# Kernel optimization log

Measured on AMD Instinct MI355X. Metric: run time of the kernel, lower is better.

The kernel has to match this reference:

```python
import jax, jax.numpy as jnp
import numpy as np

N = 100000
E = 1600000
IN_FEATS = 128
OUT_FEATS = 64


def setup_inputs() -> dict:
    key = jax.random.key(0)
    ks = jax.random.split(key, 8)
    node_feat = jax.random.normal(ks[0], (N, IN_FEATS), dtype=jnp.float32)
    edge_feat = jax.random.normal(ks[1], (E, 1), dtype=jnp.float32)
    # Linear params (PyTorch Linear: y = x @ W^T + b; we store W already transposed as [in, out])
    W_node = jax.random.normal(ks[2], (IN_FEATS, OUT_FEATS), dtype=jnp.float32) / np.sqrt(IN_FEATS)
    b_node = jax.random.normal(ks[3], (OUT_FEATS,), dtype=jnp.float32) * 0.01
    W_edge = jax.random.normal(ks[4], (1, OUT_FEATS), dtype=jnp.float32)
    b_edge = jax.random.normal(ks[5], (OUT_FEATS,), dtype=jnp.float32) * 0.01
    src = jax.random.randint(ks[6], (E,), 0, N, dtype=jnp.int32)
    dst = jax.random.randint(ks[7], (E,), 0, N, dtype=jnp.int32)
    return {"node_feat": node_feat, "edge_feat": edge_feat, "W_node": W_node,
            "b_node": b_node, "W_edge": W_edge, "b_edge": b_edge,
            "src": src, "dst": dst}


def reference(node_feat, edge_feat, W_node, b_node, W_edge, b_edge, src, dst):
    n_nodes = node_feat.shape[0]
    # node linear: h = node_fc(node_feat)  -> [N, out]
    h = node_feat @ W_node + b_node
    # edge linear: he = edge_fc(edge_feat) -> [E, out]
    he = edge_feat @ W_edge + b_edge
    # u_add_e: m = h[src] + he  (gather + add)  -> [E, out]
    m = h[src] + he
    # mean aggregate over destination nodes (segment mean; 0 for isolated nodes, as in DGL)
    msg_sum = jax.ops.segment_sum(m, dst, num_segments=n_nodes)  # [N, out]
    deg = jax.ops.segment_sum(jnp.ones((dst.shape[0],), dtype=m.dtype), dst, num_segments=n_nodes)  # [N]
    h_new = msg_sum / jnp.maximum(deg, 1.0)[:, None]
    return h_new
```

## Files before the change

kernel.cpp:

```cpp
#include <hip/hip_runtime.h>

#define IN_F 128
#define OUT_F 64
#define BSH 6
#define BNODES 64
#define NBMAX 1600
#define MSC 4096
#define CAPB 2048

typedef __attribute__((ext_vector_type(8))) short short8;
typedef __attribute__((ext_vector_type(4))) float f32x4;

static __device__ __forceinline__ unsigned short f2bf(float f) {
    unsigned u = __float_as_uint(f);
    u += 0x7FFF + ((u >> 16) & 1);
    return (unsigned short)(u >> 16);
}

__global__ void prep(const float* __restrict__ W, unsigned short* __restrict__ Wt,
                     int* __restrict__ gcur, int nb) {
    int i = blockIdx.x * 256 + threadIdx.x;
    if (i < OUT_F * IN_F) {
        int o = i >> 7, k = i & 127;
        Wt[i] = f2bf(W[k * OUT_F + o]);
    }
    if (i < nb) gcur[i] = i * CAPB;
}

__global__ __launch_bounds__(256) void node_linear_mfma(const float* __restrict__ nf,
                                                        const unsigned short* __restrict__ Wt,
                                                        const float* __restrict__ bn,
                                                        unsigned short* __restrict__ h16,
                                                        int n_nodes, int n_tiles) {
    const int lane = threadIdx.x & 63;
    const int wid  = threadIdx.x >> 6;
    const int l15  = lane & 15;
    const int kq   = lane >> 4;

    short8 bfrag[4][4];
#pragma unroll
    for (int c = 0; c < 4; ++c)
#pragma unroll
        for (int ks = 0; ks < 4; ++ks)
            bfrag[c][ks] = *(const short8*)&Wt[(c * 16 + l15) * IN_F + ks * 32 + kq * 8];

    float bv[4];
#pragma unroll
    for (int c = 0; c < 4; ++c) bv[c] = bn[c * 16 + l15];

    for (int tile = blockIdx.x * 4 + wid; tile < n_tiles; tile += gridDim.x * 4) {
        int arow = tile * 16 + l15;
        if (arow >= n_nodes) arow = n_nodes - 1;
        const float* rp = nf + (size_t)arow * IN_F + kq * 8;

        f32x4 acc[4];
#pragma unroll
        for (int c = 0; c < 4; ++c) acc[c] = (f32x4){bv[c], bv[c], bv[c], bv[c]};

#pragma unroll
        for (int ks = 0; ks < 4; ++ks) {
            float4 x0 = *(const float4*)(rp + ks * 32);
            float4 x1 = *(const float4*)(rp + ks * 32 + 4);
            short8 af;
            af[0] = (short)f2bf(x0.x); af[1] = (short)f2bf(x0.y);
            af[2] = (short)f2bf(x0.z); af[3] = (short)f2bf(x0.w);
            af[4] = (short)f2bf(x1.x); af[5] = (short)f2bf(x1.y);
            af[6] = (short)f2bf(x1.z); af[7] = (short)f2bf(x1.w);
#pragma unroll
            for (int c = 0; c < 4; ++c)
                acc[c] = __builtin_amdgcn_mfma_f32_16x16x32_bf16(af, bfrag[c][ks], acc[c], 0, 0, 0);
        }

#pragma unroll
        for (int j = 0; j < 4; ++j) {
            int node = tile * 16 + kq * 4 + j;
            if (node < n_nodes) {
#pragma unroll
                for (int c = 0; c < 4; ++c)
                    h16[(size_t)node * OUT_F + c * 16 + l15] = f2bf(acc[c][j]);
            }
        }
    }
}

__global__ __launch_bounds__(1024) void multisplit(const int* __restrict__ src,
                                                   const int* __restrict__ dst,
                                                   const float* __restrict__ ef,
                                                   int* __restrict__ gcur,
                                                   int2* __restrict__ es,
                                                   int n_edges, int nb) {
    __shared__ int2 stage[MSC];
    __shared__ unsigned short sbuck[MSC];
    __shared__ int lhist[NBMAX];
    __shared__ int lcur[NBMAX];
    __shared__ int gbase[NBMAX];
    __shared__ int part[1024];

    const int t = threadIdx.x;
    const int cb = blockIdx.x * MSC;
    const int valid = min(MSC, n_edges - cb);
    if (valid <= 0) return;

    for (int i = t; i < nb; i += 1024) lhist[i] = 0;

    int   dr[4]; int sr[4]; float fr[4];
#pragma unroll
    for (int k = 0; k < 4; ++k) {
        int i = t + (k << 10);
        if (i < valid) { dr[k] = dst[cb + i]; sr[k] = src[cb + i]; fr[k] = ef[cb + i]; }
        else           { dr[k] = -1; sr[k] = 0; fr[k] = 0.f; }
    }
    __syncthreads();

#pragma unroll
    for (int k = 0; k < 4; ++k)
        if (dr[k] >= 0) atomicAdd(&lhist[dr[k] >> BSH], 1);
    __syncthreads();

    {
        const int b0 = t << 1;
        int v0 = (b0 < nb) ? lhist[b0] : 0;
        int v1 = (b0 + 1 < nb) ? lhist[b0 + 1] : 0;
        int s = v0 + v1;
        part[t] = s;
        __syncthreads();
        for (int off = 1; off < 1024; off <<= 1) {
            int x = (t >= off) ? part[t - off] : 0;
            __syncthreads();
            part[t] += x;
            __syncthreads();
        }
        int excl = part[t] - s;
        if (b0 < nb)     lcur[b0] = excl;
        if (b0 + 1 < nb) lcur[b0 + 1] = excl + v0;
    }
    __syncthreads();

    for (int b = t; b < nb; b += 1024) {
        int c = lhist[b];
        gbase[b] = c ? atomicAdd(&gcur[b], c) : 0;
    }
    __syncthreads();

#pragma unroll
    for (int k = 0; k < 4; ++k) {
        if (dr[k] >= 0) {
            int b = dr[k] >> BSH;
            int p = atomicAdd(&lcur[b], 1);
            int dl = dr[k] & (BNODES - 1);
            stage[p] = make_int2((dl << 17) | sr[k], __float_as_int(fr[k]));
            sbuck[p] = (unsigned short)b;
        }
    }
    __syncthreads();

    for (int i = t; i < valid; i += 1024) {
        int b = sbuck[i];
        int pos = gbase[b] + (i - (lcur[b] - lhist[b]));
        if (pos < (b + 1) * CAPB) es[pos] = stage[i];
    }
}

__global__ __launch_bounds__(512, 8) void aggregate(const unsigned short* __restrict__ h16,
                                                    const int2* __restrict__ es,
                                                    const int* __restrict__ gcur,
                                                    const float* __restrict__ We,
                                                    const float* __restrict__ be,
                                                    float* __restrict__ out, int n_nodes) {
    __shared__ int2 stage[CAPB];
    __shared__ int lhist8[8][BNODES];
    __shared__ int lhist[BNODES];
    __shared__ int lbase[BNODES];
    __shared__ int lcur[BNODES];

    const int t = threadIdx.x;
    const int bkt = blockIdx.x;
    const int s0 = bkt * CAPB;
    int cnt = gcur[bkt] - s0;
    if (cnt > CAPB) cnt = CAPB;

    ((int*)lhist8)[t] = 0;
    __syncthreads();

    const int wv = t >> 6;
    int2 er[4];
#pragma unroll
    for (int k = 0; k < 4; ++k) {
        int i = t + (k << 9);
        if (i < cnt) er[k] = es[s0 + i];
    }
#pragma unroll
    for (int k = 0; k < 4; ++k) {
        int i = t + (k << 9);
        if (i < cnt) atomicAdd(&lhist8[wv][((unsigned)er[k].x) >> 17], 1);
    }
    __syncthreads();

    if (t < BNODES) {
        int v = 0;
#pragma unroll
        for (int w = 0; w < 8; ++w) v += lhist8[w][t];
        lhist[t] = v;
        int s = v;
#pragma unroll
        for (int off = 1; off < 64; off <<= 1) {
            int x = __shfl_up(s, off, 64);
            if (t >= off) s += x;
        }
        lbase[t] = s - v;
        lcur[t]  = s - v;
    }
    __syncthreads();

#pragma unroll
    for (int k = 0; k < 4; ++k) {
        int i = t + (k << 9);
        if (i < cnt) {
            int b = ((unsigned)er[k].x) >> 17;
            int p = atomicAdd(&lcur[b], 1);
            stage[p] = er[k];
        }
    }
    __syncthreads();

    const int lane = t & 63;
    const int q    = lane >> 4;
    const int o4e  = (lane & 15) << 2;
    const float4 we4 = *(const float4*)&We[o4e];
    const float4 be4 = *(const float4*)&be[o4e];

#pragma unroll
    for (int g = 0; g < 2; ++g) {
        const int dl0 = (wv << 3) + (g << 2);
        int jb[4], dgv[4];
#pragma unroll
        for (int u = 0; u < 4; ++u) { jb[u] = lbase[dl0 + u]; dgv[u] = lhist[dl0 + u]; }
        float4 ac[4];
        float sx[4];
#pragma unroll
        for (int u = 0; u < 4; ++u) { ac[u] = make_float4(0.f, 0.f, 0.f, 0.f); sx[u] = 0.f; }
        int jm = max(max(dgv[0], dgv[1]), max(dgv[2], dgv[3]));

        for (int j = 0; j < jm; j += 4) {
            int2 e[4];
#pragma unroll
            for (int u = 0; u < 4; ++u)
                e[u] = (j + q < dgv[u]) ? stage[jb[u] + j + q] : make_int2(0, 0);
            uint2 h[4];
#pragma unroll
            for (int u = 0; u < 4; ++u)
                h[u] = (j + q < dgv[u]) ? *(const uint2*)&h16[((size_t)(e[u].x & 0x1FFFF) << 6) + o4e]
                                        : make_uint2(0u, 0u);
#pragma unroll
            for (int u = 0; u < 4; ++u) {
                ac[u].x += __uint_as_float(h[u].x << 16);
                ac[u].y += __uint_as_float(h[u].x & 0xFFFF0000u);
                ac[u].z += __uint_as_float(h[u].y << 16);
                ac[u].w += __uint_as_float(h[u].y & 0xFFFF0000u);
                sx[u]   += __int_as_float(e[u].y);
            }
        }

#define RED_(v) { v += __shfl_xor(v, 16, 64); v += __shfl_xor(v, 32, 64); }
#pragma unroll
        for (int u = 0; u < 4; ++u) {
            RED_(ac[u].x) RED_(ac[u].y) RED_(ac[u].z) RED_(ac[u].w) RED_(sx[u])
        }
#undef RED_
        if (q == 0) {
#pragma unroll
            for (int u = 0; u < 4; ++u) {
                int node = (bkt << BSH) + dl0 + u;
                if (node < n_nodes) {
                    float4 r = make_float4(0.f, 0.f, 0.f, 0.f);
                    int dg = dgv[u];
                    if (dg > 0) {
                        float dgf = (float)dg, inv = 1.f / dgf;
                        r.x = (ac[u].x + we4.x * sx[u] + dgf * be4.x) * inv;
                        r.y = (ac[u].y + we4.y * sx[u] + dgf * be4.y) * inv;
                        r.z = (ac[u].z + we4.z * sx[u] + dgf * be4.z) * inv;
                        r.w = (ac[u].w + we4.w * sx[u] + dgf * be4.w) * inv;
                    }
                    *(float4*)&out[((size_t)node << 6) + o4e] = r;
                }
            }
        }
    }
}

extern "C" void kernel_launch(void* const* d_in, const int* in_sizes, int n_in,
                              void* d_out, int out_size, void* d_ws, size_t ws_size,
                              hipStream_t stream) {
    const float* nf  = (const float*)d_in[0];
    const float* ef  = (const float*)d_in[1];
    const float* Wn  = (const float*)d_in[2];
    const float* bn  = (const float*)d_in[3];
    const float* We  = (const float*)d_in[4];
    const float* be  = (const float*)d_in[5];
    const int*   src = (const int*)d_in[6];
    const int*   dst = (const int*)d_in[7];
    float* out = (float*)d_out;

    const int n_nodes = in_sizes[0] / IN_F;
    const int n_edges = in_sizes[6];
    const int nb = (n_nodes + BNODES - 1) >> BSH;
    const int n_tiles = (n_nodes + 15) / 16;

    char* w = (char*)d_ws;
    unsigned short* h16 = (unsigned short*)w; w += (size_t)n_nodes * OUT_F * sizeof(unsigned short);
    int2* es  = (int2*)w; w += (size_t)nb * CAPB * sizeof(int2);
    int* gcur = (int*)w;  w += (size_t)NBMAX * sizeof(int);
    unsigned short* Wt = (unsigned short*)w; w += (size_t)OUT_F * IN_F * sizeof(unsigned short);

    prep<<<32, 256, 0, stream>>>(Wn, Wt, gcur, nb);
    node_linear_mfma<<<782, 256, 0, stream>>>(nf, Wt, bn, h16, n_nodes, n_tiles);
    multisplit<<<(n_edges + MSC - 1) / MSC, 1024, 0, stream>>>(src, dst, ef, gcur, es, n_edges, nb);
    aggregate<<<nb, 512, 0, stream>>>(h16, es, gcur, We, be, out, n_nodes);
}
```

Measured before the change: 91.47 us.

## Fuse node linear and multisplit into one horizontally-fused launch

Merges the node-linear MFMA kernel and the edge multisplit kernel into a single 1024-thread launch. Each block does one 256-node slice of the linear and one edge chunk, with the order alternated by block parity so memory and compute phases overlap across blocks. The multisplit prefix scan changes from a Hillis-Steele LDS scan with many barriers to wave shuffles plus a small cross-wave pass, and one barrier is dropped. The aggregate inner loop is also unrolled by two. The cost is reloading W fragments per tile and a larger per-block LDS footprint, with the node-linear waves running inside 1024-thread blocks.

New measurement: 105.9 us. 15.7% more time.

```diff
diff --git a/kernel.cpp b/kernel.cpp
--- a/kernel.cpp
+++ b/kernel.cpp
@@ -27,83 +27,70 @@
     if (i < nb) gcur[i] = i * CAPB;
 }
 
-__global__ __launch_bounds__(256) void node_linear_mfma(const float* __restrict__ nf,
-                                                        const unsigned short* __restrict__ Wt,
-                                                        const float* __restrict__ bn,
-                                                        unsigned short* __restrict__ h16,
-                                                        int n_nodes, int n_tiles) {
-    const int lane = threadIdx.x & 63;
-    const int wid  = threadIdx.x >> 6;
-    const int l15  = lane & 15;
-    const int kq   = lane >> 4;
-
-    short8 bfrag[4][4];
-#pragma unroll
-    for (int c = 0; c < 4; ++c)
-#pragma unroll
-        for (int ks = 0; ks < 4; ++ks)
-            bfrag[c][ks] = *(const short8*)&Wt[(c * 16 + l15) * IN_F + ks * 32 + kq * 8];
-
-    float bv[4];
-#pragma unroll
-    for (int c = 0; c < 4; ++c) bv[c] = bn[c * 16 + l15];
-
-    for (int tile = blockIdx.x * 4 + wid; tile < n_tiles; tile += gridDim.x * 4) {
-        int arow = tile * 16 + l15;
-        if (arow >= n_nodes) arow = n_nodes - 1;
-        const float* rp = nf + (size_t)arow * IN_F + kq * 8;
-
-        f32x4 acc[4];
-#pragma unroll
-        for (int c = 0; c < 4; ++c) acc[c] = (f32x4){bv[c], bv[c], bv[c], bv[c]};
-
+__device__ __forceinline__ void do_nl(int bid, int t,
+        const float* __restrict__ nf, const unsigned short* __restrict__ Wt,
+        const float* __restrict__ bn, unsigned short* __restrict__ h16,
+        int n_nodes, int n_tiles) {
+    const int wv = t >> 6, lane = t & 63;
+    const int l15 = lane & 15, kq = lane >> 4;
+    const int tile = bid * 16 + wv;
+    if (tile >= n_tiles) return;
+
+    int arow = tile * 16 + l15;
+    if (arow >= n_nodes) arow = n_nodes - 1;
+    const float* rp = nf + (size_t)arow * IN_F + kq * 8;
+
+    short8 af[4];
+#pragma unroll
+    for (int ks = 0; ks < 4; ++ks) {
+        float4 x0 = *(const float4*)(rp + ks * 32);
+        float4 x1 = *(const float4*)(rp + ks * 32 + 4);
+        short8 a;
+        a[0] = (short)f2bf(x0.x); a[1] = (short)f2bf(x0.y);
+        a[2] = (short)f2bf(x0.z); a[3] = (short)f2bf(x0.w);
+        a[4] = (short)f2bf(x1.x); a[5] = (short)f2bf(x1.y);
+        a[6] = (short)f2bf(x1.z); a[7] = (short)f2bf(x1.w);
+        af[ks] = a;
+    }
+
+#pragma unroll
+    for (int c = 0; c < 4; ++c) {
+        float b = bn[c * 16 + l15];
+        f32x4 acc = (f32x4){b, b, b, b};
 #pragma unroll
         for (int ks = 0; ks < 4; ++ks) {
-            float4 x0 = *(const float4*)(rp + ks * 32);
-            float4 x1 = *(const float4*)(rp + ks * 32 + 4);
-            short8 af;
-            af[0] = (short)f2bf(x0.x); af[1] = (short)f2bf(x0.y);
-            af[2] = (short)f2bf(x0.z); af[3] = (short)f2bf(x0.w);
-            af[4] = (short)f2bf(x1.x); af[5] = (short)f2bf(x1.y);
-            af[6] = (short)f2bf(x1.z); af[7] = (short)f2bf(x1.w);
-#pragma unroll
-            for (int c = 0; c < 4; ++c)
-                acc[c] = __builtin_amdgcn_mfma_f32_16x16x32_bf16(af, bfrag[c][ks], acc[c], 0, 0, 0);
-        }
-
+            short8 bf = *(const short8*)&Wt[(c * 16 + l15) * IN_F + ks * 32 + kq * 8];
+            acc = __builtin_amdgcn_mfma_f32_16x16x32_bf16(af[ks], bf, acc, 0, 0, 0);
+        }
 #pragma unroll
         for (int j = 0; j < 4; ++j) {
             int node = tile * 16 + kq * 4 + j;
-            if (node < n_nodes) {
-#pragma unroll
-                for (int c = 0; c < 4; ++c)
-                    h16[(size_t)node * OUT_F + c * 16 + l15] = f2bf(acc[c][j]);
-            }
-        }
-    }
-}
-
-__global__ __launch_bounds__(1024) void multisplit(const int* __restrict__ src,
-                                                   const int* __restrict__ dst,
-                                                   const float* __restrict__ ef,
-                                                   int* __restrict__ gcur,
-                                                   int2* __restrict__ es,
-                                                   int n_edges, int nb) {
-    __shared__ int2 stage[MSC];
-    __shared__ unsigned short sbuck[MSC];
-    __shared__ int lhist[NBMAX];
-    __shared__ int lcur[NBMAX];
-    __shared__ int gbase[NBMAX];
-    __shared__ int part[1024];
-
-    const int t = threadIdx.x;
-    const int cb = blockIdx.x * MSC;
+            if (node < n_nodes)
+                h16[(size_t)node * OUT_F + c * 16 + l15] = f2bf(acc[j]);
+        }
+    }
+}
+
+struct MsLds {
+    int2 stage[MSC];
+    unsigned short sbuck[MSC];
+    int lhist[NBMAX];
+    int lcur[NBMAX];
+    int gbase[NBMAX];
+    int wtot[16];
+};
+
+__device__ __forceinline__ void do_ms(MsLds& L, int bid, int t,
+        const int* __restrict__ src, const int* __restrict__ dst,
+        const float* __restrict__ ef, int* __restrict__ gcur,
+        int2* __restrict__ es, int n_edges, int nb) {
+    const int cb = bid * MSC;
     const int valid = min(MSC, n_edges - cb);
     if (valid <= 0) return;
 
-    for (int i = t; i < nb; i += 1024) lhist[i] = 0;
-
-    int   dr[4]; int sr[4]; float fr[4];
+    for (int i = t; i < nb; i += 1024) L.lhist[i] = 0;
+
+    int dr[4]; int sr[4]; float fr[4];
 #pragma unroll
     for (int k = 0; k < 4; ++k) {
         int i = t + (k << 10);
@@ -114,50 +101,77 @@
 
 #pragma unroll
     for (int k = 0; k < 4; ++k)
-        if (dr[k] >= 0) atomicAdd(&lhist[dr[k] >> BSH], 1);
-    __syncthreads();
-
-    {
-        const int b0 = t << 1;
-        int v0 = (b0 < nb) ? lhist[b0] : 0;
-        int v1 = (b0 + 1 < nb) ? lhist[b0 + 1] : 0;
-        int s = v0 + v1;
-        part[t] = s;
-        __syncthreads();
-        for (int off = 1; off < 1024; off <<= 1) {
-            int x = (t >= off) ? part[t - off] : 0;
-            __syncthreads();
-            part[t] += x;
-            __syncthreads();
-        }
-        int excl = part[t] - s;
-        if (b0 < nb)     lcur[b0] = excl;
-        if (b0 + 1 < nb) lcur[b0 + 1] = excl + v0;
-    }
+        if (dr[k] >= 0) atomicAdd(&L.lhist[dr[k] >> BSH], 1);
+    __syncthreads();
+
+    const int wv = t >> 6, lane = t & 63;
+    const int b0 = t << 1;
+    int v0 = (b0 < nb) ? L.lhist[b0] : 0;
+    int v1 = (b0 + 1 < nb) ? L.lhist[b0 + 1] : 0;
+    int s = v0 + v1;
+    int sc = s;
+#pragma unroll
+    for (int off = 1; off < 64; off <<= 1) {
+        int x = __shfl_up(sc, off, 64);
+        if (lane >= off) sc += x;
+    }
+    if (lane == 63) L.wtot[wv] = sc;
+    __syncthreads();
+    if (t < 16) {
+        int v = L.wtot[t];
+        int s2 = v;
+#pragma unroll
+        for (int off = 1; off < 16; off <<= 1) {
+            int x = __shfl_up(s2, off, 64);
+            if (t >= off) s2 += x;
+        }
+        L.wtot[t] = s2 - v;
+    }
+    __syncthreads();
+    int excl = L.wtot[wv] + (sc - s);
+    if (b0 < nb)     L.lcur[b0] = excl;
+    if (b0 + 1 < nb) L.lcur[b0 + 1] = excl + v0;
     __syncthreads();
 
     for (int b = t; b < nb; b += 1024) {
-        int c = lhist[b];
-        gbase[b] = c ? atomicAdd(&gcur[b], c) : 0;
-    }
-    __syncthreads();
-
+        int c = L.lhist[b];
+        L.gbase[b] = c ? atomicAdd(&gcur[b], c) : 0;
+    }
 #pragma unroll
     for (int k = 0; k < 4; ++k) {
         if (dr[k] >= 0) {
             int b = dr[k] >> BSH;
-            int p = atomicAdd(&lcur[b], 1);
+            int p = atomicAdd(&L.lcur[b], 1);
             int dl = dr[k] & (BNODES - 1);
-            stage[p] = make_int2((dl << 17) | sr[k], __float_as_int(fr[k]));
-            sbuck[p] = (unsigned short)b;
+            L.stage[p] = make_int2((dl << 17) | sr[k], __float_as_int(fr[k]));
+            L.sbuck[p] = (unsigned short)b;
         }
     }
     __syncthreads();
 
     for (int i = t; i < valid; i += 1024) {
-        int b = sbuck[i];
-        int pos = gbase[b] + (i - (lcur[b] - lhist[b]));
-        if (pos < (b + 1) * CAPB) es[pos] = stage[i];
+        int b = L.sbuck[i];
+        int pos = L.gbase[b] + (i - (L.lcur[b] - L.lhist[b]));
+        if (pos < (b + 1) * CAPB) es[pos] = L.stage[i];
+    }
+}
+
+__global__ __launch_bounds__(1024, 8) void fused_ms_nl(
+        const float* __restrict__ nf, const unsigned short* __restrict__ Wt,
+        const float* __restrict__ bn, unsigned short* __restrict__ h16,
+        int n_nodes, int n_tiles,
+        const int* __restrict__ src, const int* __restrict__ dst,
+        const float* __restrict__ ef, int* __restrict__ gcur,
+        int2* __restrict__ es, int n_edges, int nb) {
+    __shared__ MsLds L;
+    const int bid = blockIdx.x;
+    const int t = threadIdx.x;
+    if (bid & 1) {
+        do_nl(bid, t, nf, Wt, bn, h16, n_nodes, n_tiles);
+        do_ms(L, bid, t, src, dst, ef, gcur, es, n_edges, nb);
+    } else {
+        do_ms(L, bid, t, src, dst, ef, gcur, es, n_edges, nb);
+        do_nl(bid, t, nf, Wt, bn, h16, n_nodes, n_tiles);
     }
 }
 
@@ -241,6 +255,7 @@
         for (int u = 0; u < 4; ++u) { ac[u] = make_float4(0.f, 0.f, 0.f, 0.f); sx[u] = 0.f; }
         int jm = max(max(dgv[0], dgv[1]), max(dgv[2], dgv[3]));
 
+#pragma unroll 2
         for (int j = 0; j < jm; j += 4) {
             int2 e[4];
 #pragma unroll
@@ -312,8 +327,12 @@
     int* gcur = (int*)w;  w += (size_t)NBMAX * sizeof(int);
     unsigned short* Wt = (unsigned short*)w; w += (size_t)OUT_F * IN_F * sizeof(unsigned short);
 
+    const int n_ms = (n_edges + MSC - 1) / MSC;
+    const int n_nl = (n_tiles + 15) / 16;
+    const int grid = n_ms > n_nl ? n_ms : n_nl;
+
     prep<<<32, 256, 0, stream>>>(Wn, Wt, gcur, nb);
-    node_linear_mfma<<<782, 256, 0, stream>>>(nf, Wt, bn, h16, n_nodes, n_tiles);
-    multisplit<<<(n_edges + MSC - 1) / MSC, 1024, 0, stream>>>(src, dst, ef, gcur, es, n_edges, nb);
+    fused_ms_nl<<<grid, 1024, 0, stream>>>(nf, Wt, bn, h16, n_nodes, n_tiles,
+                                           src, dst, ef, gcur, es, n_edges, nb);
     aggregate<<<nb, 512, 0, stream>>>(h16, es, gcur, We, be, out, n_nodes);
 }
```
